# Optimization experiments

Measured on AMD Instinct MI355X. Metric: run time of the kernel, lower is better.

The kernel has to match this reference:

```python
import jax, jax.numpy as jnp
import numpy as np

N = 50000      # nodes across the batched graph
E = 400000     # edges
F_IN = 128     # gnn_input_size
H = 3          # num_head
D = 64         # gnn_hidden_size
G = 64         # graphs in batch
P = 64         # pattern_input_size
NEG_GAT = 0.2  # GATv2Conv leaky_relu slope (dgl default)
NEG = 0.01     # nn.LeakyReLU default slope


def setup_inputs() -> dict:
    key = jax.random.key(0)
    ks = jax.random.split(key, 32)
    rn = lambda k, s, sc=0.05: jax.random.normal(k, s, dtype=jnp.float32) * sc
    HD = H * D
    return {
        "inputs": rn(ks[0], (N, F_IN), 1.0),
        "src": jax.random.randint(ks[1], (E,), 0, N),
        "dst": jax.random.randint(ks[2], (E,), 0, N),
        "graph_ids": jnp.sort(jax.random.randint(ks[3], (N,), 0, G)),
        "p1": rn(ks[4], (G, P), 1.0),
        "p2": rn(ks[5], (G, P), 1.0),
        "p3": rn(ks[6], (G, P), 1.0),
        # GATv2 layer params: fc_src, fc_dst, attn vector, bias
        "W1s": rn(ks[7], (F_IN, HD)), "W1d": rn(ks[8], (F_IN, HD)),
        "a1": rn(ks[9], (H, D)), "b1": rn(ks[10], (HD,)),
        "W2s": rn(ks[11], (HD, HD)), "W2d": rn(ks[12], (HD, HD)),
        "a2": rn(ks[13], (H, D)), "b2": rn(ks[14], (HD,)),
        "W3s": rn(ks[15], (HD, HD)), "W3d": rn(ks[16], (HD, HD)),
        "a3": rn(ks[17], (H, D)), "b3": rn(ks[18], (HD,)),
        # pattern branch (forward only uses ex_layer1 for all three inputs)
        "Wex": rn(ks[19], (P, 32)), "bex": rn(ks[20], (32,)),
        "Wpat": rn(ks[21], (96, P)), "bpat": rn(ks[22], (P,)),
        # classifier head
        "Wc1": rn(ks[23], (D + P, 64)), "bc1": rn(ks[24], (64,)),
        "Wc2": rn(ks[25], (64, 32)), "bc2": rn(ks[26], (32,)),
        "Wc3": rn(ks[27], (32, 2)), "bc3": rn(ks[28], (2,)),
    }


def _gatv2(x, src, dst, Ws, Wd, attn, bias):
    # dgl GATv2Conv (share_weights=False): e = a . leaky_relu(Ws x_u + Wd x_v)
    fs = (x @ Ws).reshape(N, H, D)
    fd = (x @ Wd).reshape(N, H, D)
    e = jax.nn.leaky_relu(fs[src] + fd[dst], NEG_GAT)            # [E,H,D]
    logits = jnp.einsum('ehd,hd->eh', e, attn)                   # [E,H]
    m = jax.ops.segment_max(logits, dst, num_segments=N)         # [N,H]
    m = jnp.where(jnp.isfinite(m), m, 0.0)                       # nodes w/o in-edges
    ex = jnp.exp(logits - m[dst])
    denom = jax.ops.segment_sum(ex, dst, num_segments=N)         # [N,H]
    alpha = ex / jnp.maximum(denom, 1e-9)[dst]                   # edge softmax
    out = jax.ops.segment_sum(alpha[:, :, None] * fs[src], dst, num_segments=N)
    return out + bias.reshape(1, H, D)                           # [N,H,D]


def reference(inputs, src, dst, graph_ids, p1, p2, p3,
              W1s, W1d, a1, b1, W2s, W2d, a2, b2, W3s, W3d, a3, b3,
              Wex, bex, Wpat, bpat, Wc1, bc1, Wc2, bc2, Wc3, bc3):
    h = _gatv2(inputs, src, dst, W1s, W1d, a1, b1).reshape(N, H * D)
    h = _gatv2(h, src, dst, W2s, W2d, a2, b2).reshape(N, H * D)
    h = _gatv2(h, src, dst, W3s, W3d, a3, b3).mean(axis=1)       # [N,D]
    # dgl.mean_nodes: per-graph mean over nodes
    sums = jax.ops.segment_sum(h, graph_ids, num_segments=G)
    cnts = jax.ops.segment_sum(jnp.ones((N,), h.dtype), graph_ids, num_segments=G)
    gnn_out = sums / jnp.maximum(cnts, 1.0)[:, None]             # [G,D]
    # pattern branch (ex_layer1 applied to all three, as in source)
    px = jnp.concatenate([p1 @ Wex + bex, p2 @ Wex + bex, p3 @ Wex + bex], axis=1)
    px = jax.nn.leaky_relu(px @ Wpat + bpat, NEG)                # [G,P]
    x = jnp.concatenate([gnn_out, px], axis=1)                   # [G,D+P]
    x = jax.nn.leaky_relu(x @ Wc1 + bc1, NEG)
    x = jax.nn.leaky_relu(x @ Wc2 + bc2, NEG)
    return x @ Wc3 + bc3                                         # [G,2]
```

## Files before the change

### kernel.cpp

```cpp
#include <hip/hip_runtime.h>
#include <cstdint>
#include <cstddef>

#define NN 50000
#define EE 400000
#define FIN 128
#define HH 3
#define DD 64
#define GG 64
#define PP 64
#define HD 192

typedef short bf16x8 __attribute__((ext_vector_type(8)));
typedef float f32x4 __attribute__((ext_vector_type(4)));
typedef unsigned int u32x2 __attribute__((ext_vector_type(2)));

__device__ inline int wsumi(int v) {
#pragma unroll
    for (int m = 32; m > 0; m >>= 1) v += __shfl_xor(v, m, 64);
    return v;
}

__device__ inline float bf2f(unsigned short u) {
    union { unsigned int i; float f; } x; x.i = ((unsigned int)u) << 16; return x.f;
}
__device__ inline unsigned short f2bf(float f) {
    union { float f; unsigned int i; } x; x.f = f;
    unsigned int r = x.i + 0x7FFFu + ((x.i >> 16) & 1u);
    return (unsigned short)(r >> 16);
}

__device__ inline void unp2(unsigned int w, float& lo, float& hi) {
    union { unsigned int i; float f; } x;
    x.i = w << 16;          lo = x.f;
    x.i = w & 0xFFFF0000u;  hi = x.f;
}
__device__ inline void load4(const unsigned short* p, float* o) {
    u32x2 w = *(const u32x2*)p;
    unp2(w[0], o[0], o[1]);
    unp2(w[1], o[2], o[3]);
}

__device__ inline void loadrow(const unsigned short* __restrict__ FS, int u, int col,
                               float f[3][4]) {
    size_t bu = (size_t)u * HD + col;
#pragma unroll
    for (int h = 0; h < 3; h++) load4(&FS[bu + h * 64], f[h]);
}

__global__ void k_count(const int* __restrict__ dst, int* __restrict__ counts) {
    int e = blockIdx.x * 256 + threadIdx.x;
    if (e < EE) atomicAdd(&counts[dst[e]], 1);
}

__global__ void k_scan_block(const int* __restrict__ in, int* __restrict__ out,
                             int* __restrict__ bsums) {
    __shared__ int tmp[1024];
    int tid = threadIdx.x;
    int i = blockIdx.x * 1024 + tid;
    int v = (i < NN) ? in[i] : 0;
    tmp[tid] = v;
    __syncthreads();
    for (int off = 1; off < 1024; off <<= 1) {
        int t = (tid >= off) ? tmp[tid - off] : 0;
        __syncthreads();
        tmp[tid] += t;
        __syncthreads();
    }
    if (i < NN) out[i] = tmp[tid] - v;
    if (tid == 1023) bsums[blockIdx.x] = tmp[1023];
}

__global__ void k_scan_add(int* __restrict__ row_ptr, const int* __restrict__ bsums, int nb) {
    __shared__ int sbase;
    int tid = threadIdx.x;
    if (tid < 64) {
        int v = (tid < blockIdx.x) ? bsums[tid] : 0;
        v = wsumi(v);
        if (tid == 0) sbase = v;
    }
    __syncthreads();
    int i = blockIdx.x * 1024 + tid;
    if (i < NN) row_ptr[i] += sbase;
    else if (i == NN) row_ptr[NN] = EE;
}

__global__ void k_scatter(const int* __restrict__ src, const int* __restrict__ dst,
                          const int* __restrict__ row_ptr, int* __restrict__ cursor,
                          int* __restrict__ csr_src) {
    int e = blockIdx.x * 256 + threadIdx.x;
    if (e >= EE) return;
    int v = dst[e];
    int pos = row_ptr[v] + atomicAdd(&cursor[v], 1);
    csr_src[pos] = src[e];
}

__device__ inline void pack_one(const float* __restrict__ W, unsigned short* __restrict__ WP,
                                int id, int Kc) {
    int lane = id & 63;
    int kc = (id >> 6) % Kc;
    int ct = (id >> 6) / Kc;
    int n = ct * 16 + (lane & 15);
    int kb = kc * 32 + (lane >> 4) * 8;
#pragma unroll
    for (int j = 0; j < 8; j++)
        WP[(unsigned)id * 8 + j] = f2bf(W[(unsigned)(kb + j) * HD + n]);
}

#define IDS128 (12 * 4 * 64)
#define IDS192 (12 * 6 * 64)
__global__ void k_pack_all(const float* W1s, const float* W1d,
                           const float* W2s, const float* W2d,
                           const float* W3s, const float* W3d,
                           unsigned short* P1s, unsigned short* P1d,
                           unsigned short* P2s, unsigned short* P2d,
                           unsigned short* P3s, unsigned short* P3d) {
    int idx = blockIdx.x * 256 + threadIdx.x;
    if (idx < IDS128) { pack_one(W1s, P1s, idx, 4); return; }
    idx -= IDS128;
    if (idx < IDS128) { pack_one(W1d, P1d, idx, 4); return; }
    idx -= IDS128;
    if (idx < IDS192) { pack_one(W2s, P2s, idx, 6); return; }
    idx -= IDS192;
    if (idx < IDS192) { pack_one(W2d, P2d, idx, 6); return; }
    idx -= IDS192;
    if (idx < IDS192) { pack_one(W3s, P3s, idx, 6); return; }
    idx -= IDS192;
    if (idx < IDS192) { pack_one(W3d, P3d, idx, 6); return; }
}

template <int K, bool BF16IN>
__global__ __launch_bounds__(256) void k_gemm_mfma(const void* __restrict__ Xin,
                                                   const unsigned short* __restrict__ WPs,
                                                   const unsigned short* __restrict__ WPd,
                                                   unsigned short* __restrict__ FS,
                                                   unsigned short* __restrict__ FD) {
    constexpr int Kc = K / 32;
    __shared__ unsigned short xs[16][K + 8];
    __shared__ unsigned short cs[16][392];
    int tid = threadIdx.x;
    int row0 = blockIdx.x * 16;
    if (BF16IN) {
        const unsigned short* XB = (const unsigned short*)Xin;
        for (int c = tid; c < 16 * K / 8; c += 256) {
            int r = c / (K / 8), kk = (c - r * (K / 8)) * 8;
            *(bf16x8*)&xs[r][kk] = *(const bf16x8*)&XB[(unsigned)((row0 + r) * K + kk)];
        }
    } else {
        const float* X = (const float*)Xin;
        for (int idx = tid; idx < 16 * K; idx += 256) {
            int r = idx / K, k = idx - r * K;
            xs[r][k] = f2bf(X[(unsigned)((row0 + r) * K + k)]);
        }
    }
    __syncthreads();

    int lane = tid & 63, wv = tid >> 6;
    int m = lane & 15, quad = lane >> 4;
    f32x4 acc[6];
#pragma unroll
    for (int t = 0; t < 6; t++) acc[t] = (f32x4){0.f, 0.f, 0.f, 0.f};

    for (int kc = 0; kc < Kc; kc++) {
        bf16x8 a = *(const bf16x8*)&xs[m][kc * 32 + quad * 8];
#pragma unroll
        for (int t = 0; t < 6; t++) {
            int ct = wv * 6 + t;
            const unsigned short* wp = (ct < 12) ? WPs : WPd;
            int c = (ct < 12) ? ct : ct - 12;
            bf16x8 b = *(const bf16x8*)&wp[(unsigned)(((c * Kc + kc) * 64 + lane) * 8)];
            acc[t] = __builtin_amdgcn_mfma_f32_16x16x32_bf16(a, b, acc[t], 0, 0, 0);
        }
    }
#pragma unroll
    for (int t = 0; t < 6; t++) {
        int ct = wv * 6 + t;
#pragma unroll
        for (int r = 0; r < 4; r++)
            cs[quad * 4 + r][ct * 16 + m] = f2bf(acc[t][r]);
    }
    __syncthreads();
#pragma unroll
    for (int it = 0; it < 3; it++) {
        int c = tid + it * 256;
        int hm = c / 384;
        int cc = c - hm * 384;
        int row = cc / 24, ch = cc - row * 24;
        unsigned short* OUT = hm ? FD : FS;
        *(bf16x8*)&OUT[(unsigned)((row0 + row) * HD + ch * 8)] =
            *(const bf16x8*)&cs[row][hm * 192 + ch * 8];
    }
}

template <bool FINAL>
__global__ __launch_bounds__(256) void k_node_gat(const int* __restrict__ row_ptr,
                                                  const int* __restrict__ csr_src,
                                                  const unsigned short* __restrict__ FS,
                                                  const unsigned short* __restrict__ FD,
                                                  const float* __restrict__ A,
                                                  const float* __restrict__ Bv,
                                                  unsigned short* __restrict__ XB,
                                                  float* __restrict__ H64) {
    int tid = threadIdx.x;
    int grp = tid >> 4, sub = tid & 15;
    int node = blockIdx.x * 16 + grp;
    int col = sub * 4;

    float a[3][4];
#pragma unroll
    for (int h = 0; h < 3; h++) {
        f32x4 av = *(const f32x4*)&A[h * 64 + col];
#pragma unroll
        for (int j = 0; j < 4; j++) a[h][j] = av[j];
    }

    int lo = row_ptr[node], hi = row_ptr[node + 1];

    float g[3][4];
#pragma unroll
    for (int h = 0; h < 3; h++) load4(&FD[(size_t)node * HD + h * 64 + col], g[h]);

    float r[3][4];
#pragma unroll
    for (int h = 0; h < 3; h++)
#pragma unroll
        for (int j = 0; j < 4; j++) r[h][j] = 0.f;
    float d0 = 0.f, d1 = 0.f, d2 = 0.f;

    auto accum = [&](const float f[3][4]) {
        float p0 = 0.f, p1 = 0.f, p2 = 0.f;
#pragma unroll
        for (int j = 0; j < 4; j++) {
            float s0 = f[0][j] + g[0][j]; s0 = fmaxf(s0, 0.2f * s0); p0 += s0 * a[0][j];
            float s1 = f[1][j] + g[1][j]; s1 = fmaxf(s1, 0.2f * s1); p1 += s1 * a[1][j];
            float s2 = f[2][j] + g[2][j]; s2 = fmaxf(s2, 0.2f * s2); p2 += s2 * a[2][j];
        }
#pragma unroll
        for (int m = 8; m > 0; m >>= 1) {
            p0 += __shfl_xor(p0, m, 64);
            p1 += __shfl_xor(p1, m, 64);
            p2 += __shfl_xor(p2, m, 64);
        }
        float w0 = __expf(p0), w1 = __expf(p1), w2 = __expf(p2);
#pragma unroll
        for (int j = 0; j < 4; j++) {
            r[0][j] += w0 * f[0][j];
            r[1][j] += w1 * f[1][j];
            r[2][j] += w2 * f[2][j];
        }
        d0 += w0; d1 += w1; d2 += w2;
    };

    if (hi > lo) {
        int last = hi - 1;
        float fA[3][4], fB[3][4], fC[3][4];
        loadrow(FS, csr_src[lo], col, fA);
        loadrow(FS, csr_src[lo + 1 <= last ? lo + 1 : last], col, fB);
        for (int e = lo; e < hi; e += 3) {
            int eC = e + 2 <= last ? e + 2 : last;
            int eA = e + 3 <= last ? e + 3 : last;
            int eB = e + 4 <= last ? e + 4 : last;
            int uC = csr_src[eC], uA = csr_src[eA], uB = csr_src[eB];
            loadrow(FS, uC, col, fC);
            accum(fA);
            loadrow(FS, uA, col, fA);
            if (e + 1 < hi) accum(fB);
            loadrow(FS, uB, col, fB);
            if (e + 2 < hi) accum(fC);
        }
    }

    float b[3][4];
#pragma unroll
    for (int h = 0; h < 3; h++) {
        f32x4 bv = *(const f32x4*)&Bv[h * 64 + col];
#pragma unroll
        for (int j = 0; j < 4; j++) b[h][j] = bv[j];
    }

    float q0 = fmaxf(d0, 1e-9f), q1 = fmaxf(d1, 1e-9f), q2 = fmaxf(d2, 1e-9f);
    if (FINAL) {
        f32x4 m;
#pragma unroll
        for (int j = 0; j < 4; j++)
            m[j] = (r[0][j] / q0 + b[0][j] + r[1][j] / q1 + b[1][j] +
                    r[2][j] / q2 + b[2][j]) * (1.f / 3.f);
        *(f32x4*)&H64[(size_t)node * 64 + col] = m;
    } else {
        float qq[3] = {q0, q1, q2};
#pragma unroll
        for (int h = 0; h < 3; h++) {
            unsigned short o0 = f2bf(r[h][0] / qq[h] + b[h][0]);
            unsigned short o1 = f2bf(r[h][1] / qq[h] + b[h][1]);
            unsigned short o2 = f2bf(r[h][2] / qq[h] + b[h][2]);
            unsigned short o3 = f2bf(r[h][3] / qq[h] + b[h][3]);
            u32x2 w;
            w[0] = (unsigned)o0 | ((unsigned)o1 << 16);
            w[1] = (unsigned)o2 | ((unsigned)o3 << 16);
            *(u32x2*)&XB[(size_t)node * HD + h * 64 + col] = w;
        }
    }
}

__global__ __launch_bounds__(256) void k_graph_mean(const float* __restrict__ H64,
                                                    const int* __restrict__ gids,
                                                    float* __restrict__ gsum,
                                                    int* __restrict__ gcnt) {
    int g = blockIdx.x >> 2, q = blockIdx.x & 3;
    int lo, hi;
    {
        int a = 0, b = NN;
        while (a < b) { int m = (a + b) >> 1; if (gids[m] < g) a = m + 1; else b = m; }
        lo = a;
        b = NN;
        while (a < b) { int m = (a + b) >> 1; if (gids[m] < g + 1) a = m + 1; else b = m; }
        hi = a;
    }
    int len = hi - lo;
    int qlen = (len + 3) >> 2;
    int s = lo + q * qlen;
    int e = s + qlen; if (e > hi) e = hi;
    int lane = threadIdx.x & 63, wv = threadIdx.x >> 6;

    float acc = 0.f;
    for (int v = s + wv; v < e; v += 4)
        acc += H64[(size_t)v * 64 + lane];
    __shared__ float red[4][64];
    red[wv][lane] = acc;
    __syncthreads();
    if (wv == 0) {
        float t = red[0][lane] + red[1][lane] + red[2][lane] + red[3][lane];
        if (e > s) {
            atomicAdd(&gsum[g * 64 + lane], t);
            if (lane == 0) atomicAdd(&gcnt[g], e - s);
        }
    }
}

__global__ __launch_bounds__(128) void k_head(const float* __restrict__ gsum, const int* __restrict__ gcnt,
                                              const float* __restrict__ p1, const float* __restrict__ p2,
                                              const float* __restrict__ p3,
                                              const float* __restrict__ Wex, const float* __restrict__ bex,
                                              const float* __restrict__ Wpat, const float* __restrict__ bpat,
                                              const float* __restrict__ Wc1, const float* __restrict__ bc1,
                                              const float* __restrict__ Wc2, const float* __restrict__ bc2,
                                              const float* __restrict__ Wc3, const float* __restrict__ bc3,
                                              float* __restrict__ out) {
    int g = blockIdx.x;
    int tid = threadIdx.x;
    __shared__ float pbuf[192];
    __shared__ float ex[96], xc[128], t1[64], t2[32];

    if (tid < 64)       pbuf[tid] = p1[g * 64 + tid];
    else if (tid < 128) pbuf[tid] = p2[g * 64 + tid - 64];
    if (tid < 64)       pbuf[128 + tid] = p3[g * 64 + tid];
    if (tid >= 64 && tid < 128)
        xc[tid - 64] = gsum[g * 64 + tid - 64] / fmaxf((float)gcnt[g], 1.f);
    __syncthreads();
    if (tid < 96) {
        int jj = tid & 31;
        const float* pp = &pbuf[(tid >> 5) * 64];
        float acc = bex[jj];
        for (int k = 0; k < 64; k++) acc += pp[k] * Wex[k * 32 + jj];
        ex[tid] = acc;
    }
    __syncthreads();
    if (tid < 64) {
        float acc = bpat[tid];
        for (int k = 0; k < 96; k++) acc += ex[k] * Wpat[k * 64 + tid];
        xc[64 + tid] = acc > 0.f ? acc : 0.01f * acc;
    }
    __syncthreads();
    if (tid < 64) {
        float acc = bc1[tid];
        for (int k = 0; k < 128; k++) acc += xc[k] * Wc1[k * 64 + tid];
        t1[tid] = acc > 0.f ? acc : 0.01f * acc;
    }
    __syncthreads();
    if (tid < 32) {
        float acc = bc2[tid];
        for (int k = 0; k < 64; k++) acc += t1[k] * Wc2[k * 32 + tid];
        t2[tid] = acc > 0.f ? acc : 0.01f * acc;
    }
    __syncthreads();
    if (tid < 2) {
        float acc = bc3[tid];
        for (int k = 0; k < 32; k++) acc += t2[k] * Wc3[k * 2 + tid];
        out[g * 2 + tid] = acc;
    }
}

extern "C" void kernel_launch(void* const* d_in, const int* in_sizes, int n_in,
                              void* d_out, int out_size, void* d_ws, size_t ws_size,
                              hipStream_t stream) {
    const float* X0  = (const float*)d_in[0];
    const int*   src = (const int*)d_in[1];
    const int*   dst = (const int*)d_in[2];
    const int*   gid = (const int*)d_in[3];
    const float* p1  = (const float*)d_in[4];
    const float* p2  = (const float*)d_in[5];
    const float* p3  = (const float*)d_in[6];
    const float* W1s = (const float*)d_in[7],  *W1d = (const float*)d_in[8];
    const float* a1  = (const float*)d_in[9],  *b1  = (const float*)d_in[10];
    const float* W2s = (const float*)d_in[11], *W2d = (const float*)d_in[12];
    const float* a2  = (const float*)d_in[13], *b2  = (const float*)d_in[14];
    const float* W3s = (const float*)d_in[15], *W3d = (const float*)d_in[16];
    const float* a3  = (const float*)d_in[17], *b3  = (const float*)d_in[18];
    const float* Wex = (const float*)d_in[19], *bex = (const float*)d_in[20];
    const float* Wpat= (const float*)d_in[21], *bpat= (const float*)d_in[22];
    const float* Wc1 = (const float*)d_in[23], *bc1 = (const float*)d_in[24];
    const float* Wc2 = (const float*)d_in[25], *bc2 = (const float*)d_in[26];
    const float* Wc3 = (const float*)d_in[27], *bc3 = (const float*)d_in[28];
    float* out = (float*)d_out;

    char* ws = (char*)d_ws;
    size_t off = 0;
    auto alloc = [&](size_t bytes) -> char* {
        char* p = ws + off;
        off = (off + bytes + 255) & ~(size_t)255;
        return p;
    };
    unsigned short* FS = (unsigned short*)alloc((size_t)NN * HD * 2);
    unsigned short* FD = (unsigned short*)alloc((size_t)NN * HD * 2);
    unsigned short* XB = (unsigned short*)alloc((size_t)NN * HD * 2);
    float*          H64= (float*)alloc((size_t)NN * 64 * 4);
    unsigned short* P1s = (unsigned short*)alloc((size_t)192 * 192 * 2);
    unsigned short* P1d = (unsigned short*)alloc((size_t)192 * 192 * 2);
    unsigned short* P2s = (unsigned short*)alloc((size_t)192 * 192 * 2);
    unsigned short* P2d = (unsigned short*)alloc((size_t)192 * 192 * 2);
    unsigned short* P3s = (unsigned short*)alloc((size_t)192 * 192 * 2);
    unsigned short* P3d = (unsigned short*)alloc((size_t)192 * 192 * 2);
    int* row_ptr = (int*)alloc((size_t)(NN + 1) * 4);
    int* csr_src = (int*)alloc((size_t)EE * 4);
    int* bsums   = (int*)alloc(64 * 4);
    char* zbase = ws + off;
    int*   counts = (int*)alloc((size_t)NN * 4);
    int*   cursor = (int*)alloc((size_t)NN * 4);
    float* gsum   = (float*)alloc((size_t)GG * 64 * 4);
    int*   gcnt   = (int*)alloc((size_t)GG * 4);
    size_t zbytes = (size_t)((ws + off) - zbase);

    hipMemsetAsync(zbase, 0, zbytes, stream);

    int ebl = (EE + 255) / 256;
    int nb  = (NN + 1023) / 1024;
    k_count<<<ebl, 256, 0, stream>>>(dst, counts);
    k_scan_block<<<nb, 1024, 0, stream>>>(counts, row_ptr, bsums);
    k_scan_add<<<nb, 1024, 0, stream>>>(row_ptr, bsums, nb);
    k_scatter<<<ebl, 256, 0, stream>>>(src, dst, row_ptr, cursor, csr_src);
    {
        int total = 2 * IDS128 + 4 * IDS192;
        k_pack_all<<<(total + 255) / 256, 256, 0, stream>>>(W1s, W1d, W2s, W2d, W3s, W3d,
                                                            P1s, P1d, P2s, P2d, P3s, P3d);
    }

    int gblk = NN / 16;
    int nblk = NN / 16;

    k_gemm_mfma<128, false><<<gblk, 256, 0, stream>>>(X0, P1s, P1d, FS, FD);
    k_node_gat<false><<<nblk, 256, 0, stream>>>(row_ptr, csr_src, FS, FD, a1, b1, XB, nullptr);
    k_gemm_mfma<192, true><<<gblk, 256, 0, stream>>>(XB, P2s, P2d, FS, FD);
    k_node_gat<false><<<nblk, 256, 0, stream>>>(row_ptr, csr_src, FS, FD, a2, b2, XB, nullptr);
    k_gemm_mfma<192, true><<<gblk, 256, 0, stream>>>(XB, P3s, P3d, FS, FD);
    k_node_gat<true><<<nblk, 256, 0, stream>>>(row_ptr, csr_src, FS, FD, a3, b3, nullptr, H64);

    k_graph_mean<<<GG * 4, 256, 0, stream>>>(H64, gid, gsum, gcnt);
    k_head<<<GG, 128, 0, stream>>>(gsum, gcnt, p1, p2, p3, Wex, bex, Wpat, bpat,
                                   Wc1, bc1, Wc2, bc2, Wc3, bc3, out);
}
```

Measured before the change: 385.0 us.

## Process 64 rows per GEMM block to reuse packed weight fragments

The MFMA projection GEMM now handles 64 node rows per block instead of 16. Each wave loads its six weight fragments once per K-chunk and applies them to four 16-row sub-tiles, so global weight traffic per output row drops by about four times. The input tile and output staging buffer share one LDS allocation, fp32 input loads are vectorized, and rows past the end are clamped or masked. The cost is 96 accumulator registers per thread, a larger LDS footprint, and four times fewer blocks, which may lower occupancy.

Result: no change. 377.7 us, median of 2 (-1.9%).

```diff
diff --git a/kernel.cpp b/kernel.cpp
--- a/kernel.cpp
+++ b/kernel.cpp
@@ -136,59 +136,81 @@
                                                    unsigned short* __restrict__ FS,
                                                    unsigned short* __restrict__ FD) {
     constexpr int Kc = K / 32;
-    __shared__ unsigned short xs[16][K + 8];
-    __shared__ unsigned short cs[16][392];
+    __shared__ unsigned short smem[64 * 392];
+    unsigned short (*xs)[K + 8] = (unsigned short (*)[K + 8])smem;
+    unsigned short (*cs)[392]   = (unsigned short (*)[392])smem;
     int tid = threadIdx.x;
-    int row0 = blockIdx.x * 16;
+    int row0 = blockIdx.x * 64;
+
     if (BF16IN) {
         const unsigned short* XB = (const unsigned short*)Xin;
-        for (int c = tid; c < 16 * K / 8; c += 256) {
+        for (int c = tid; c < 64 * K / 8; c += 256) {
             int r = c / (K / 8), kk = (c - r * (K / 8)) * 8;
-            *(bf16x8*)&xs[r][kk] = *(const bf16x8*)&XB[(unsigned)((row0 + r) * K + kk)];
+            int row = row0 + r; if (row > NN - 1) row = NN - 1;
+            *(bf16x8*)&xs[r][kk] = *(const bf16x8*)&XB[(unsigned)(row * K + kk)];
         }
     } else {
         const float* X = (const float*)Xin;
-        for (int idx = tid; idx < 16 * K; idx += 256) {
-            int r = idx / K, k = idx - r * K;
-            xs[r][k] = f2bf(X[(unsigned)((row0 + r) * K + k)]);
+        for (int c = tid; c < 64 * K / 4; c += 256) {
+            int r = c / (K / 4), k4 = (c - r * (K / 4)) * 4;
+            int row = row0 + r; if (row > NN - 1) row = NN - 1;
+            f32x4 v = *(const f32x4*)&X[(unsigned)(row * K + k4)];
+            xs[r][k4 + 0] = f2bf(v[0]);
+            xs[r][k4 + 1] = f2bf(v[1]);
+            xs[r][k4 + 2] = f2bf(v[2]);
+            xs[r][k4 + 3] = f2bf(v[3]);
         }
     }
     __syncthreads();
 
     int lane = tid & 63, wv = tid >> 6;
     int m = lane & 15, quad = lane >> 4;
-    f32x4 acc[6];
-#pragma unroll
-    for (int t = 0; t < 6; t++) acc[t] = (f32x4){0.f, 0.f, 0.f, 0.f};
+    f32x4 acc[4][6];
+#pragma unroll
+    for (int s = 0; s < 4; s++)
+#pragma unroll
+        for (int t = 0; t < 6; t++) acc[s][t] = (f32x4){0.f, 0.f, 0.f, 0.f};
 
     for (int kc = 0; kc < Kc; kc++) {
-        bf16x8 a = *(const bf16x8*)&xs[m][kc * 32 + quad * 8];
+        bf16x8 b[6];
 #pragma unroll
         for (int t = 0; t < 6; t++) {
             int ct = wv * 6 + t;
             const unsigned short* wp = (ct < 12) ? WPs : WPd;
             int c = (ct < 12) ? ct : ct - 12;
-            bf16x8 b = *(const bf16x8*)&wp[(unsigned)(((c * Kc + kc) * 64 + lane) * 8)];
-            acc[t] = __builtin_amdgcn_mfma_f32_16x16x32_bf16(a, b, acc[t], 0, 0, 0);
-        }
-    }
-#pragma unroll
-    for (int t = 0; t < 6; t++) {
-        int ct = wv * 6 + t;
-#pragma unroll
-        for (int r = 0; r < 4; r++)
-            cs[quad * 4 + r][ct * 16 + m] = f2bf(acc[t][r]);
-    }
-    __syncthreads();
-#pragma unroll
-    for (int it = 0; it < 3; it++) {
+            b[t] = *(const bf16x8*)&wp[(unsigned)(((c * Kc + kc) * 64 + lane) * 8)];
+        }
+#pragma unroll
+        for (int s = 0; s < 4; s++) {
+            bf16x8 a = *(const bf16x8*)&xs[s * 16 + m][kc * 32 + quad * 8];
+#pragma unroll
+            for (int t = 0; t < 6; t++)
+                acc[s][t] = __builtin_amdgcn_mfma_f32_16x16x32_bf16(a, b[t], acc[s][t], 0, 0, 0);
+        }
+    }
+    __syncthreads();
+#pragma unroll
+    for (int s = 0; s < 4; s++)
+#pragma unroll
+        for (int t = 0; t < 6; t++) {
+            int ct = wv * 6 + t;
+#pragma unroll
+            for (int r = 0; r < 4; r++)
+                cs[s * 16 + quad * 4 + r][ct * 16 + m] = f2bf(acc[s][t][r]);
+        }
+    __syncthreads();
+#pragma unroll
+    for (int it = 0; it < 12; it++) {
         int c = tid + it * 256;
-        int hm = c / 384;
-        int cc = c - hm * 384;
+        int hm = c / 1536;
+        int cc = c - hm * 1536;
         int row = cc / 24, ch = cc - row * 24;
-        unsigned short* OUT = hm ? FD : FS;
-        *(bf16x8*)&OUT[(unsigned)((row0 + row) * HD + ch * 8)] =
-            *(const bf16x8*)&cs[row][hm * 192 + ch * 8];
+        int grow = row0 + row;
+        if (grow < NN) {
+            unsigned short* OUT = hm ? FD : FS;
+            *(bf16x8*)&OUT[(unsigned)(grow * HD + ch * 8)] =
+                *(const bf16x8*)&cs[row][hm * 192 + ch * 8];
+        }
     }
 }
 
@@ -454,7 +476,7 @@
                                                             P1s, P1d, P2s, P2d, P3s, P3d);
     }
 
-    int gblk = NN / 16;
+    int gblk = (NN + 63) / 64;
     int nblk = NN / 16;
 
     k_gemm_mfma<128, false><<<gblk, 256, 0, stream>>>(X0, P1s, P1d, FS, FD);
```
